# Optimization experiments

Measured on AMD Instinct MI355X. Metric: run time of the kernel, lower is better.

The kernel has to match this reference:

```python
import jax, jax.numpy as jnp
import numpy as np

# Config matching init_kwargs (single TP rank: local heads == total heads)
HID = 1024
NH = 16      # query heads
NKV = 4      # kv heads (GQA)
HD = 64      # head_dim
B = 2
S = 2048
SCALE = 1.0 / HD ** 0.5


def setup_inputs() -> dict:
    key = jax.random.key(0)
    k1, k2, k3 = jax.random.split(key, 3)
    qkv_out = (NH + 2 * NKV) * HD  # 1536
    return {
        "hidden_states": jax.random.normal(k1, (B, S, HID), dtype=jnp.float32),
        "W_qkv": jax.random.normal(k2, (HID, qkv_out), dtype=jnp.float32) * 0.02,
        "W_o": jax.random.normal(k3, (HID, HID), dtype=jnp.float32) * 0.02,
    }


def reference(hidden_states, W_qkv, W_o):
    b, s, _ = hidden_states.shape
    rep = NH // NKV  # GQA repeat factor (repeat_interleave: q head h uses kv group h // rep)

    qkv = hidden_states @ W_qkv  # [B, S, (NH+2*NKV)*HD]
    q, k, v = jnp.split(qkv, [NH * HD, (NH + NKV) * HD], axis=-1)

    # [B, heads, S, HD]
    q = q.reshape(b, s, NH, HD).transpose(0, 2, 1, 3)
    k = k.reshape(b, s, NKV, HD).transpose(0, 2, 1, 3)
    v = v.reshape(b, s, NKV, HD).transpose(0, 2, 1, 3)

    # Group query heads by shared kv head instead of repeat_interleaving K/V in memory.
    qg = q.reshape(b, NKV, rep, s, HD)  # head h = g*rep + r  <=>  kv group g = h // rep
    scores = jnp.einsum("bgrqd,bgkd->bgrqk", qg, k) * SCALE  # [B, NKV, rep, S, S]

    # Causal mask (prefill path: kv_cache is None, seq_len > 1)
    causal = jnp.triu(jnp.ones((s, s), dtype=bool), k=1)
    scores = jnp.where(causal, jnp.finfo(scores.dtype).min, scores)

    attn = jax.nn.softmax(scores, axis=-1)
    out = jnp.einsum("bgrqk,bgkd->bgrqd", attn, v)  # [B, NKV, rep, S, HD]
    out = out.reshape(b, NH, s, HD).transpose(0, 2, 1, 3).reshape(b, s, NH * HD)
    return out @ W_o  # [B, S, HID]
```

## Files before the change

### kernel.cpp

```cpp
#include <hip/hip_runtime.h>
#include <stdint.h>

using u16 = unsigned short;
using u32 = unsigned int;

typedef __attribute__((ext_vector_type(8))) short short8;
typedef __attribute__((ext_vector_type(4))) float f32x4;
typedef __attribute__((ext_vector_type(16))) float f32x16;

__device__ __forceinline__ u16 f2bf(float f) {
  u32 u = __builtin_bit_cast(u32, f);
  u = (u + 0x7fffu + ((u >> 16) & 1u)) >> 16;
  return (u16)u;
}

__device__ __forceinline__ u32 cvtpk(float lo, float hi) {
  u32 r;
  asm("v_cvt_pk_bf16_f32 %0, %1, %2" : "=v"(r) : "v"(lo), "v"(hi));
  return r;
}

__device__ __forceinline__ short8 ld16(const u16* p) {
  uint4 v = *(const uint4*)p;
  union { uint4 u; short8 s; } c; c.u = v; return c.s;
}

__device__ __forceinline__ short8 ld16s(const u16* p) {
  uint4 v = *(const uint4*)p;
  union { uint4 u; short8 s; } c; c.u = v; return c.s;
}

__device__ __forceinline__ void gload_lds16(const void* g, void* l) {
  __builtin_amdgcn_global_load_lds(
      (const __attribute__((address_space(1))) void*)g,
      (__attribute__((address_space(3))) void*)l, 16, 0, 0);
}

__device__ __forceinline__ f32x16 mfma32(short8 a, short8 b, f32x16 c) {
  return __builtin_amdgcn_mfma_f32_32x32x16_bf16(a, b, c, 0, 0, 0);
}

__global__ __launch_bounds__(256) void k_f32_to_bf16(const float* __restrict__ in,
                                                     u16* __restrict__ out, int n4) {
  int i = blockIdx.x * 256 + threadIdx.x;
  if (i >= n4) return;
  float4 v = ((const float4*)in)[i];
  ushort4 o;
  o.x = f2bf(v.x); o.y = f2bf(v.y); o.z = f2bf(v.z); o.w = f2bf(v.w);
  ((ushort4*)out)[i] = o;
}

__global__ __launch_bounds__(256) void k_transpose_bf16(const float* __restrict__ in,
                                                        u16* __restrict__ out, int R, int C) {
  __shared__ float tile[32][33];
  int c0 = blockIdx.x * 32, r0 = blockIdx.y * 32;
  int tx = threadIdx.x & 31, ty = threadIdx.x >> 5;
#pragma unroll
  for (int i = 0; i < 4; ++i) {
    int r = ty + 8 * i;
    tile[r][tx] = in[(size_t)(r0 + r) * C + c0 + tx];
  }
  __syncthreads();
#pragma unroll
  for (int i = 0; i < 4; ++i) {
    int r = ty + 8 * i;
    out[(size_t)(c0 + r) * R + r0 + tx] = f2bf(tile[tx][r]);
  }
}

template <int EPI>
__global__ __launch_bounds__(256, 2) void k_gemm(
    const u16* __restrict__ A, const u16* __restrict__ BT, int M, int N, int K,
    u16* __restrict__ qb, u16* __restrict__ kb, u16* __restrict__ vbT,
    float* __restrict__ out) {
  __shared__ __align__(16) u16 As[2][128 * 64];
  __shared__ __align__(16) u16 Bs[2][128 * 64];
  const int t = threadIdx.x;
  const int l = t & 63;
  const int wid = t >> 6;
  const int wr = wid >> 1, wc = wid & 1;
  const int lr = l & 15, lg = l >> 4;
  const int cpx = (int)gridDim.x >> 3;
  const int nb = (blockIdx.x & 7) * cpx + ((int)blockIdx.x >> 3);
  const int ntile = N >> 7;
  const int mt = nb / ntile, nt = nb % ntile;
  const int m0 = mt << 7, n0 = nt << 7;

  f32x4 zero = {0.f, 0.f, 0.f, 0.f};
  f32x4 acc[4][4];
#pragma unroll
  for (int i = 0; i < 4; ++i)
#pragma unroll
    for (int j = 0; j < 4; ++j) acc[i][j] = zero;

  const u16* Ab = A + (size_t)m0 * K;
  const u16* Bb = BT + (size_t)n0 * K;
  const int nkt = K >> 6;

  auto STAGE = [&](int kt, int bsel) {
    const u16* Ak = Ab + kt * 64;
    const u16* Bk = Bb + kt * 64;
#pragma unroll
    for (int i = 0; i < 4; ++i) {
      int o16 = i * 256 + t;
      int row = o16 >> 3, c = o16 & 7;
      int sc = c ^ (row & 7);
      gload_lds16(Ak + (size_t)row * K + sc * 8, &As[bsel][o16 * 8]);
    }
#pragma unroll
    for (int i = 0; i < 4; ++i) {
      int o16 = i * 256 + t;
      int row = o16 >> 3, c = o16 & 7;
      int sc = c ^ (row & 7);
      gload_lds16(Bk + (size_t)row * K + sc * 8, &Bs[bsel][o16 * 8]);
    }
  };

  STAGE(0, 0);
  asm volatile("s_waitcnt vmcnt(0)" ::: "memory");
  __builtin_amdgcn_s_barrier();

  for (int kt = 0; kt < nkt; ++kt) {
    const int cur = kt & 1;
    if (kt + 1 < nkt) STAGE(kt + 1, cur ^ 1);
#pragma unroll
    for (int ks = 0; ks < 2; ++ks) {
      short8 a[4], b[4];
#pragma unroll
      for (int mi = 0; mi < 4; ++mi) {
        int row = wr * 64 + mi * 16 + lr;
        int c = (ks * 4 + lg) ^ (row & 7);
        a[mi] = ld16(&As[cur][(row * 8 + c) * 8]);
      }
#pragma unroll
      for (int ni = 0; ni < 4; ++ni) {
        int row = wc * 64 + ni * 16 + lr;
        int c = (ks * 4 + lg) ^ (row & 7);
        b[ni] = ld16(&Bs[cur][(row * 8 + c) * 8]);
      }
#pragma unroll
      for (int mi = 0; mi < 4; ++mi)
#pragma unroll
        for (int ni = 0; ni < 4; ++ni)
          acc[mi][ni] = __builtin_amdgcn_mfma_f32_16x16x32_bf16(a[mi], b[ni], acc[mi][ni], 0, 0, 0);
    }
    asm volatile("s_waitcnt vmcnt(0)" ::: "memory");
    __builtin_amdgcn_s_barrier();
    asm volatile("" ::: "memory");
  }

#pragma unroll
  for (int mi = 0; mi < 4; ++mi) {
#pragma unroll
    for (int ni = 0; ni < 4; ++ni) {
#pragma unroll
      for (int r = 0; r < 4; ++r) {
        float v = acc[mi][ni][r];
        int m = m0 + wr * 64 + mi * 16 + 4 * lg + r;
        int n = n0 + wc * 64 + ni * 16 + lr;
        if (EPI == 0) {
          int bb = m >> 11, s = m & 2047;
          int tau = s >> 5, i32e = s & 31;
          if (n < 1024) {
            int h = n >> 6, d = n & 63;
            int kc = d >> 4, hi2 = (d >> 3) & 1, e = d & 7;
            qb[((size_t)(bb * 16 + h)) * 131072 +
               (size_t)((tau * 4 + kc) * 64 + (hi2 << 5 | i32e)) * 8 + e] = f2bf(v * 0.18033688f);
          } else if (n < 1280) {
            int g = (n - 1024) >> 6, d = n & 63;
            int kc = d >> 4, hi2 = (d >> 3) & 1, e = d & 7;
            kb[((size_t)(bb * 4 + g)) * 131072 +
               (size_t)((tau * 4 + kc) * 64 + (hi2 << 5 | i32e)) * 8 + e] = f2bf(v);
          } else {
            int g = (n - 1280) >> 6, dT = n & 63;
            int c = (s >> 4) & 1, hi2 = (s >> 3) & 1, e = s & 7;
            int dd = dT >> 5, i32v = dT & 31;
            vbT[((size_t)(bb * 4 + g)) * 131072 +
                (size_t)(((tau * 2 + dd) * 2 + c) * 64 + (hi2 << 5 | i32v)) * 8 + e] = f2bf(v);
          }
        } else {
          out[(size_t)m * N + n] = v;
        }
      }
    }
  }
}

__global__ __launch_bounds__(256, 2) void k_attn(const u16* __restrict__ qbuf,
                                                 const u16* __restrict__ kbuf,
                                                 const u16* __restrict__ vbuf,
                                                 u16* __restrict__ attn) {
  __shared__ __align__(16) u16 Ks[2][4096];
  __shared__ __align__(16) u16 Vs[2][4096];
  const int t = threadIdx.x;
  const int l = t & 63, wid = t >> 6;
  const int i32 = l & 31, hi = l >> 5;
  const int id = blockIdx.x;
  const int bh = id >> 4;
  const int T = (id & 15) ^ (((id >> 8) & 1) ? 15 : 0);
  const int b = bh >> 4, h = bh & 15, g = h >> 2;
  const int q0 = T * 128 + wid * 32;
  const int nblkw = (q0 >> 6) + 1;
  const int nmax = 2 * T + 2;

  const u16* qp = qbuf + ((size_t)(b * 16 + h)) * 131072;
  const u16* kp = kbuf + ((size_t)(b * 4 + g)) * 131072;
  const u16* vp = vbuf + ((size_t)(b * 4 + g)) * 131072;

  short8 qf[4];
#pragma unroll
  for (int kc = 0; kc < 4; ++kc)
    qf[kc] = ld16(qp + ((size_t)((q0 >> 5) * 4 + kc) * 64 + l) * 8);

  f32x16 z16 = {0.f, 0.f, 0.f, 0.f, 0.f, 0.f, 0.f, 0.f,
                0.f, 0.f, 0.f, 0.f, 0.f, 0.f, 0.f, 0.f};
  f32x16 o[2];
  o[0] = z16; o[1] = z16;
  float mrun = -1e30f, lsum = 0.f;

  auto STAGE = [&](int n, int bsel) {
    const u16* kblk = kp + (size_t)n * 4096;
    const u16* vblk = vp + (size_t)n * 4096;
    gload_lds16(kblk + t * 8, &Ks[bsel][t * 8]);
    gload_lds16(kblk + (256 + t) * 8, &Ks[bsel][(256 + t) * 8]);
    gload_lds16(vblk + t * 8, &Vs[bsel][t * 8]);
    gload_lds16(vblk + (256 + t) * 8, &Vs[bsel][(256 + t) * 8]);
  };

  STAGE(0, 0);
  asm volatile("s_waitcnt vmcnt(0)" ::: "memory");
  __builtin_amdgcn_s_barrier();

  int cur = 0;
  for (int n = 0; n < nmax; ++n) {
    if (n + 1 < nmax) STAGE(n + 1, cur ^ 1);
    if (n < nblkw) {
      const int kv0 = n * 64;
      short8 kf[2][4];
#pragma unroll
      for (int mf = 0; mf < 2; ++mf)
#pragma unroll
        for (int kc = 0; kc < 4; ++kc)
          kf[mf][kc] = ld16s(&Ks[cur][((mf * 4 + kc) * 64 + l) * 8]);

      f32x16 sc[2];
      __builtin_amdgcn_s_setprio(1);
      sc[0] = mfma32(kf[0][0], qf[0], z16);
      sc[1] = mfma32(kf[1][0], qf[0], z16);
#pragma unroll
      for (int kc = 1; kc < 4; ++kc) {
        sc[0] = mfma32(kf[0][kc], qf[kc], sc[0]);
        sc[1] = mfma32(kf[1][kc], qf[kc], sc[1]);
      }
      __builtin_amdgcn_s_setprio(0);

      if (n == nblkw - 1) {
        const int iloc = (q0 - kv0) + i32;
#pragma unroll
        for (int mf = 0; mf < 2; ++mf)
#pragma unroll
          for (int R = 0; R < 16; ++R) {
            int j = 32 * mf + (R & 3) + 8 * (R >> 2) + 4 * hi;
            if (j > iloc) sc[mf][R] = -1e30f;
          }
      }

      float mq[8];
#pragma unroll
      for (int k = 0; k < 8; ++k) {
        int mf = k >> 2, b4 = (k & 3) * 4;
        mq[k] = fmaxf(fmaxf(sc[mf][b4], sc[mf][b4 + 1]), fmaxf(sc[mf][b4 + 2], sc[mf][b4 + 3]));
      }
      float mx = fmaxf(fmaxf(fmaxf(mq[0], mq[1]), fmaxf(mq[2], mq[3])),
                       fmaxf(fmaxf(mq[4], mq[5]), fmaxf(mq[6], mq[7])));
      {
        u32 mu = __builtin_bit_cast(u32, mx);
        auto r = __builtin_amdgcn_permlane32_swap(mu, mu, false, false);
        mx = fmaxf(__builtin_bit_cast(float, (u32)r[0]), __builtin_bit_cast(float, (u32)r[1]));
      }
      if (!__all(mx - mrun <= 8.0f)) {
        float mnew = fmaxf(mrun, mx);
        float alpha = __builtin_amdgcn_exp2f(mrun - mnew);
        mrun = mnew;
        lsum *= alpha;
#pragma unroll
        for (int dd = 0; dd < 2; ++dd)
#pragma unroll
          for (int R = 0; R < 16; ++R) o[dd][R] *= alpha;
      }

      float s0 = 0.f, s1 = 0.f, s2 = 0.f, s3 = 0.f;
#pragma unroll
      for (int mf = 0; mf < 2; ++mf)
#pragma unroll
        for (int R = 0; R < 16; R += 4) {
          float p0 = __builtin_amdgcn_exp2f(sc[mf][R] - mrun);
          float p1 = __builtin_amdgcn_exp2f(sc[mf][R + 1] - mrun);
          float p2 = __builtin_amdgcn_exp2f(sc[mf][R + 2] - mrun);
          float p3 = __builtin_amdgcn_exp2f(sc[mf][R + 3] - mrun);
          sc[mf][R] = p0; sc[mf][R + 1] = p1; sc[mf][R + 2] = p2; sc[mf][R + 3] = p3;
          s0 += p0; s1 += p1; s2 += p2; s3 += p3;
        }
      lsum += (s0 + s1) + (s2 + s3);

      short8 pb[2][2];
#pragma unroll
      for (int mf = 0; mf < 2; ++mf)
#pragma unroll
        for (int c = 0; c < 2; ++c) {
          union { u32 w[4]; short8 s8; } U;
#pragma unroll
          for (int q = 0; q < 2; ++q) {
            u32 wa = cvtpk(sc[mf][8 * c + 2 * q], sc[mf][8 * c + 2 * q + 1]);
            u32 wb = cvtpk(sc[mf][8 * c + 4 + 2 * q], sc[mf][8 * c + 4 + 2 * q + 1]);
            auto r = __builtin_amdgcn_permlane32_swap(wa, wb, false, false);
            U.w[q] = (u32)r[0];
            U.w[2 + q] = (u32)r[1];
          }
          pb[mf][c] = U.s8;
        }

      short8 vf[2][2][2];
#pragma unroll
      for (int mf = 0; mf < 2; ++mf)
#pragma unroll
        for (int dd = 0; dd < 2; ++dd)
#pragma unroll
          for (int c = 0; c < 2; ++c)
            vf[dd][mf][c] = ld16s(&Vs[cur][((4 * mf + 2 * dd + c) * 64 + l) * 8]);

      __builtin_amdgcn_s_setprio(1);
#pragma unroll
      for (int mf = 0; mf < 2; ++mf)
#pragma unroll
        for (int c = 0; c < 2; ++c) {
          o[0] = mfma32(vf[0][mf][c], pb[mf][c], o[0]);
          o[1] = mfma32(vf[1][mf][c], pb[mf][c], o[1]);
        }
      __builtin_amdgcn_s_setprio(0);
    }
    asm volatile("s_waitcnt vmcnt(0)" ::: "memory");
    __builtin_amdgcn_s_barrier();
    cur ^= 1;
  }

  float tot;
  {
    u32 su = __builtin_bit_cast(u32, lsum);
    auto r = __builtin_amdgcn_permlane32_swap(su, su, false, false);
    tot = __builtin_bit_cast(float, (u32)r[0]) + __builtin_bit_cast(float, (u32)r[1]);
  }
  float inv = 1.f / tot;
  u16* ao = attn + ((size_t)(b * 2048 + q0)) * 1024 + h * 64;
#pragma unroll
  for (int dd = 0; dd < 2; ++dd) {
#pragma unroll
    for (int R = 0; R < 16; R += 2) {
      int d = dd * 32 + (R & 3) + 8 * (R >> 2) + 4 * hi;
      u32 w = cvtpk(o[dd][R] * inv, o[dd][R + 1] * inv);
      *(u32*)(ao + (size_t)i32 * 1024 + d) = w;
    }
  }
}

extern "C" void kernel_launch(void* const* d_in, const int* in_sizes, int n_in,
                              void* d_out, int out_size, void* d_ws, size_t ws_size,
                              hipStream_t stream) {
  const float* hs = (const float*)d_in[0];
  const float* wqkv = (const float*)d_in[1];
  const float* wo = (const float*)d_in[2];
  float* out = (float*)d_out;
  u16* ws = (u16*)d_ws;

  u16* hsb = ws;
  u16* wqkvT = hsb + 4194304;
  u16* woT = wqkvT + 1572864;
  u16* qb = woT + 1048576;
  u16* kb = qb + 4194304;
  u16* vb = kb + 1048576;
  u16* attn = vb + 1048576;
  (void)in_sizes; (void)n_in; (void)out_size; (void)ws_size;

  k_f32_to_bf16<<<4096, 256, 0, stream>>>(hs, hsb, 1048576);
  k_transpose_bf16<<<dim3(48, 32), 256, 0, stream>>>(wqkv, wqkvT, 1024, 1536);
  k_transpose_bf16<<<dim3(32, 32), 256, 0, stream>>>(wo, woT, 1024, 1024);
  k_gemm<0><<<384, 256, 0, stream>>>(hsb, wqkvT, 4096, 1536, 1024, qb, kb, vb, nullptr);
  k_attn<<<512, 256, 0, stream>>>(qb, kb, vb, attn);
  k_gemm<1><<<256, 256, 0, stream>>>(attn, woT, 4096, 1024, 1024, nullptr, nullptr, nullptr, out);
}
```

Baseline: 101.0 us.

## Split causal attention KV range across blocks with a combine kernel

Each query tile's KV loop is split into chunks of up to 8 blocks, so late tiles are handled by 2-4 blocks instead of one. The grid grows from 512 to 1280 blocks. Partial unnormalized outputs and per-row max/sum are written to workspace, and a new combine kernel merges them with log-sum-exp rescaling. The goal is to balance the triangular causal workload and raise occupancy, at the cost of an extra launch and extra partial-buffer traffic. The KV staging also becomes a two-deep prefetch with a partial vmcnt wait.

```diff
diff --git a/kernel.cpp b/kernel.cpp
--- a/kernel.cpp
+++ b/kernel.cpp
@@ -21,11 +21,6 @@
 }
 
 __device__ __forceinline__ short8 ld16(const u16* p) {
-  uint4 v = *(const uint4*)p;
-  union { uint4 u; short8 s; } c; c.u = v; return c.s;
-}
-
-__device__ __forceinline__ short8 ld16s(const u16* p) {
   uint4 v = *(const uint4*)p;
   union { uint4 u; short8 s; } c; c.u = v; return c.s;
 }
@@ -189,19 +184,29 @@
 __global__ __launch_bounds__(256, 2) void k_attn(const u16* __restrict__ qbuf,
                                                  const u16* __restrict__ kbuf,
                                                  const u16* __restrict__ vbuf,
-                                                 u16* __restrict__ attn) {
+                                                 u16* __restrict__ attn,
+                                                 u16* __restrict__ partO,
+                                                 float* __restrict__ partML) {
   __shared__ __align__(16) u16 Ks[2][4096];
   __shared__ __align__(16) u16 Vs[2][4096];
   const int t = threadIdx.x;
   const int l = t & 63, wid = t >> 6;
   const int i32 = l & 31, hi = l >> 5;
   const int id = blockIdx.x;
-  const int bh = id >> 4;
-  const int T = (id & 15) ^ (((id >> 8) & 1) ? 15 : 0);
+  const int bh = id / 40;
+  const int r = id % 40;
+  int T, c;
+  if (r < 4)       { T = r;                  c = 0; }
+  else if (r < 12) { T = 4 + ((r - 4) >> 1); c = (r - 4) & 1; }
+  else if (r < 24) { T = 8 + (r - 12) / 3;   c = (r - 12) % 3; }
+  else             { T = 12 + ((r - 24) >> 2); c = (r - 24) & 3; }
   const int b = bh >> 4, h = bh & 15, g = h >> 2;
   const int q0 = T * 128 + wid * 32;
-  const int nblkw = (q0 >> 6) + 1;
+  const int nblkw = 2 * T + (wid >> 1) + 1;
   const int nmax = 2 * T + 2;
+  const int c0b = 8 * c;
+  const int nEnd = (c0b + 8 < nmax) ? c0b + 8 : nmax;
+  const bool multi = (T >= 4);
 
   const u16* qp = qbuf + ((size_t)(b * 16 + h)) * 131072;
   const u16* kp = kbuf + ((size_t)(b * 4 + g)) * 131072;
@@ -227,13 +232,15 @@
     gload_lds16(vblk + (256 + t) * 8, &Vs[bsel][(256 + t) * 8]);
   };
 
-  STAGE(0, 0);
-  asm volatile("s_waitcnt vmcnt(0)" ::: "memory");
-  __builtin_amdgcn_s_barrier();
-
-  int cur = 0;
-  for (int n = 0; n < nmax; ++n) {
-    if (n + 1 < nmax) STAGE(n + 1, cur ^ 1);
+  STAGE(c0b, 0);
+  STAGE(c0b + 1, 1);
+
+  for (int n = c0b; n < nEnd; ++n) {
+    const int cur = (n - c0b) & 1;
+    if (n + 1 < nEnd) { asm volatile("s_waitcnt vmcnt(4)" ::: "memory"); }
+    else              { asm volatile("s_waitcnt vmcnt(0)" ::: "memory"); }
+    __builtin_amdgcn_s_barrier();
+
     if (n < nblkw) {
       const int kv0 = n * 64;
       short8 kf[2][4];
@@ -241,7 +248,7 @@
       for (int mf = 0; mf < 2; ++mf)
 #pragma unroll
         for (int kc = 0; kc < 4; ++kc)
-          kf[mf][kc] = ld16s(&Ks[cur][((mf * 4 + kc) * 64 + l) * 8]);
+          kf[mf][kc] = ld16(&Ks[cur][((mf * 4 + kc) * 64 + l) * 8]);
 
       f32x16 sc[2];
       __builtin_amdgcn_s_setprio(1);
@@ -275,8 +282,8 @@
                        fmaxf(fmaxf(mq[4], mq[5]), fmaxf(mq[6], mq[7])));
       {
         u32 mu = __builtin_bit_cast(u32, mx);
-        auto r = __builtin_amdgcn_permlane32_swap(mu, mu, false, false);
-        mx = fmaxf(__builtin_bit_cast(float, (u32)r[0]), __builtin_bit_cast(float, (u32)r[1]));
+        auto rr = __builtin_amdgcn_permlane32_swap(mu, mu, false, false);
+        mx = fmaxf(__builtin_bit_cast(float, (u32)rr[0]), __builtin_bit_cast(float, (u32)rr[1]));
       }
       if (!__all(mx - mrun <= 8.0f)) {
         float mnew = fmaxf(mrun, mx);
@@ -307,17 +314,17 @@
 #pragma unroll
       for (int mf = 0; mf < 2; ++mf)
 #pragma unroll
-        for (int c = 0; c < 2; ++c) {
+        for (int cc = 0; cc < 2; ++cc) {
           union { u32 w[4]; short8 s8; } U;
 #pragma unroll
           for (int q = 0; q < 2; ++q) {
-            u32 wa = cvtpk(sc[mf][8 * c + 2 * q], sc[mf][8 * c + 2 * q + 1]);
-            u32 wb = cvtpk(sc[mf][8 * c + 4 + 2 * q], sc[mf][8 * c + 4 + 2 * q + 1]);
-            auto r = __builtin_amdgcn_permlane32_swap(wa, wb, false, false);
-            U.w[q] = (u32)r[0];
-            U.w[2 + q] = (u32)r[1];
+            u32 wa = cvtpk(sc[mf][8 * cc + 2 * q], sc[mf][8 * cc + 2 * q + 1]);
+            u32 wb = cvtpk(sc[mf][8 * cc + 4 + 2 * q], sc[mf][8 * cc + 4 + 2 * q + 1]);
+            auto rr = __builtin_amdgcn_permlane32_swap(wa, wb, false, false);
+            U.w[q] = (u32)rr[0];
+            U.w[2 + q] = (u32)rr[1];
           }
-          pb[mf][c] = U.s8;
+          pb[mf][cc] = U.s8;
         }
 
       short8 vf[2][2][2];
@@ -326,41 +333,115 @@
 #pragma unroll
         for (int dd = 0; dd < 2; ++dd)
 #pragma unroll
-          for (int c = 0; c < 2; ++c)
-            vf[dd][mf][c] = ld16s(&Vs[cur][((4 * mf + 2 * dd + c) * 64 + l) * 8]);
+          for (int cc = 0; cc < 2; ++cc)
+            vf[dd][mf][cc] = ld16(&Vs[cur][((4 * mf + 2 * dd + cc) * 64 + l) * 8]);
 
       __builtin_amdgcn_s_setprio(1);
 #pragma unroll
       for (int mf = 0; mf < 2; ++mf)
 #pragma unroll
-        for (int c = 0; c < 2; ++c) {
-          o[0] = mfma32(vf[0][mf][c], pb[mf][c], o[0]);
-          o[1] = mfma32(vf[1][mf][c], pb[mf][c], o[1]);
+        for (int cc = 0; cc < 2; ++cc) {
+          o[0] = mfma32(vf[0][mf][cc], pb[mf][cc], o[0]);
+          o[1] = mfma32(vf[1][mf][cc], pb[mf][cc], o[1]);
         }
       __builtin_amdgcn_s_setprio(0);
     }
-    asm volatile("s_waitcnt vmcnt(0)" ::: "memory");
+
     __builtin_amdgcn_s_barrier();
-    cur ^= 1;
+    if (n + 2 < nEnd) STAGE(n + 2, cur);
   }
 
   float tot;
   {
     u32 su = __builtin_bit_cast(u32, lsum);
-    auto r = __builtin_amdgcn_permlane32_swap(su, su, false, false);
-    tot = __builtin_bit_cast(float, (u32)r[0]) + __builtin_bit_cast(float, (u32)r[1]);
-  }
-  float inv = 1.f / tot;
-  u16* ao = attn + ((size_t)(b * 2048 + q0)) * 1024 + h * 64;
-#pragma unroll
-  for (int dd = 0; dd < 2; ++dd) {
-#pragma unroll
-    for (int R = 0; R < 16; R += 2) {
-      int d = dd * 32 + (R & 3) + 8 * (R >> 2) + 4 * hi;
-      u32 w = cvtpk(o[dd][R] * inv, o[dd][R + 1] * inv);
-      *(u32*)(ao + (size_t)i32 * 1024 + d) = w;
-    }
-  }
+    auto rr = __builtin_amdgcn_permlane32_swap(su, su, false, false);
+    tot = __builtin_bit_cast(float, (u32)rr[0]) + __builtin_bit_cast(float, (u32)rr[1]);
+  }
+  const int row = wid * 32 + i32;
+
+  if (!multi) {
+    float inv = 1.f / tot;
+    u16* ao = attn + ((size_t)(b * 2048 + q0)) * 1024 + h * 64;
+#pragma unroll
+    for (int dd = 0; dd < 2; ++dd) {
+#pragma unroll
+      for (int R = 0; R < 16; R += 2) {
+        int d = dd * 32 + (R & 3) + 8 * (R >> 2) + 4 * hi;
+        u32 w = cvtpk(o[dd][R] * inv, o[dd][R + 1] * inv);
+        *(u32*)(ao + (size_t)i32 * 1024 + d) = w;
+      }
+    }
+  } else {
+    const int slot = bh * 40 + r;
+    u16* pO = partO + (size_t)slot * 8192;
+#pragma unroll
+    for (int dd = 0; dd < 2; ++dd) {
+#pragma unroll
+      for (int R = 0; R < 16; R += 2) {
+        int d = dd * 32 + (R & 3) + 8 * (R >> 2) + 4 * hi;
+        u32 w = cvtpk(o[dd][R], o[dd][R + 1]);
+        *(u32*)(pO + (size_t)row * 64 + d) = w;
+      }
+    }
+    if (hi == 0) {
+      float2 st; st.x = mrun; st.y = tot;
+      ((float2*)(partML + (size_t)slot * 256))[row] = st;
+    }
+  }
+}
+
+__global__ __launch_bounds__(256) void k_combine(const u16* __restrict__ partO,
+                                                 const float* __restrict__ partML,
+                                                 u16* __restrict__ attn) {
+  const int id = blockIdx.x;
+  const int bh = id >> 4, T = id & 15;
+  if (T < 4) return;
+  const int nc = (T < 8) ? 2 : (T < 12) ? 3 : 4;
+  const int r0 = (T < 8) ? 4 + 2 * (T - 4) : (T < 12) ? 12 + 3 * (T - 8) : 24 + 4 * (T - 12);
+  const int slot0 = bh * 40 + r0;
+  const int t = threadIdx.x;
+  const int row = t >> 1, d0 = (t & 1) * 32;
+
+  float mc[4], lc[4];
+#pragma unroll
+  for (int cc = 0; cc < 4; ++cc) {
+    if (cc < nc) {
+      float2 st = ((const float2*)(partML + (size_t)(slot0 + cc) * 256))[row];
+      mc[cc] = st.x; lc[cc] = st.y;
+    } else { mc[cc] = -1e30f; lc[cc] = 0.f; }
+  }
+  float mstar = fmaxf(fmaxf(mc[0], mc[1]), fmaxf(mc[2], mc[3]));
+
+  float acc[32];
+#pragma unroll
+  for (int k = 0; k < 32; ++k) acc[k] = 0.f;
+  float lst = 0.f;
+#pragma unroll
+  for (int cc = 0; cc < 4; ++cc) {
+    if (cc < nc) {
+      float w = __builtin_amdgcn_exp2f(mc[cc] - mstar);
+      lst += lc[cc] * w;
+      const u16* po = partO + (size_t)(slot0 + cc) * 8192 + (size_t)row * 64 + d0;
+#pragma unroll
+      for (int v = 0; v < 4; ++v) {
+        uint4 pk = *(const uint4*)(po + v * 8);
+        u32 ws4[4] = {pk.x, pk.y, pk.z, pk.w};
+#pragma unroll
+        for (int j = 0; j < 4; ++j) {
+          float lo = __builtin_bit_cast(float, ws4[j] << 16);
+          float hi = __builtin_bit_cast(float, ws4[j] & 0xffff0000u);
+          acc[v * 8 + 2 * j] += lo * w;
+          acc[v * 8 + 2 * j + 1] += hi * w;
+        }
+      }
+    }
+  }
+  const int b = bh >> 4, h = bh & 15;
+  float inv = 1.f / lst;
+  u16* ao = attn + ((size_t)(b * 2048 + T * 128 + row)) * 1024 + h * 64 + d0;
+#pragma unroll
+  for (int k = 0; k < 32; k += 2)
+    *(u32*)(ao + k) = cvtpk(acc[k] * inv, acc[k + 1] * inv);
 }
 
 extern "C" void kernel_launch(void* const* d_in, const int* in_sizes, int n_in,
@@ -379,12 +460,15 @@
   u16* kb = qb + 4194304;
   u16* vb = kb + 1048576;
   u16* attn = vb + 1048576;
+  u16* partO = attn + 4194304;
+  float* partML = (float*)(partO + 10485760);
   (void)in_sizes; (void)n_in; (void)out_size; (void)ws_size;
 
   k_f32_to_bf16<<<4096, 256, 0, stream>>>(hs, hsb, 1048576);
   k_transpose_bf16<<<dim3(48, 32), 256, 0, stream>>>(wqkv, wqkvT, 1024, 1536);
   k_transpose_bf16<<<dim3(32, 32), 256, 0, stream>>>(wo, woT, 1024, 1024);
   k_gemm<0><<<384, 256, 0, stream>>>(hsb, wqkvT, 4096, 1536, 1024, qb, kb, vb, nullptr);
-  k_attn<<<512, 256, 0, stream>>>(qb, kb, vb, attn);
+  k_attn<<<1280, 256, 0, stream>>>(qb, kb, vb, attn, partO, partML);
+  k_combine<<<512, 256, 0, stream>>>(partO, partML, attn);
   k_gemm<1><<<256, 256, 0, stream>>>(attn, woT, 4096, 1024, 1024, nullptr, nullptr, nullptr, out);
 }
```

Measured after the change: 103.7 us. 2.7% more time.
